# Kernel optimization log

Hardware: AMD Instinct MI355X
Metric: run time of the kernel (lower is better)

## Reference

```python
import jax, jax.numpy as jnp
import numpy as np

N_NODES = 100000
N_EDGES = 600000
F_IN = 128
HIDDEN = 128
Z_DIM = 64


def setup_inputs() -> dict:
    key = jax.random.key(0)
    ks = jax.random.split(key, 8)
    nodes = jax.random.normal(ks[0], (N_NODES, F_IN), dtype=jnp.float32)
    senders = jax.random.randint(ks[1], (N_EDGES,), 0, N_NODES, dtype=jnp.int32)
    receivers = jax.random.randint(ks[2], (N_EDGES,), 0, N_NODES, dtype=jnp.int32)
    s = lambda fan_in: 1.0 / np.sqrt(fan_in)
    W0 = jax.random.normal(ks[3], (F_IN, HIDDEN), dtype=jnp.float32) * s(F_IN)
    b0 = jnp.zeros((HIDDEN,), dtype=jnp.float32)
    W1 = jax.random.normal(ks[4], (HIDDEN, HIDDEN), dtype=jnp.float32) * s(HIDDEN)
    b1 = jnp.zeros((HIDDEN,), dtype=jnp.float32)
    Wmu = jax.random.normal(ks[5], (HIDDEN + F_IN, Z_DIM), dtype=jnp.float32) * s(HIDDEN + F_IN)
    bmu = jnp.zeros((Z_DIM,), dtype=jnp.float32)
    Wls = jax.random.normal(ks[6], (HIDDEN + F_IN, Z_DIM), dtype=jnp.float32) * s(HIDDEN + F_IN)
    bls = jnp.zeros((Z_DIM,), dtype=jnp.float32)
    return dict(nodes=nodes, senders=senders, receivers=receivers,
                W0=W0, b0=b0, W1=W1, b1=b1, Wmu=Wmu, bmu=bmu, Wls=Wls, bls=bls)


def _gc_layer(h, senders, receivers, W, b):
    """jraph.GraphConvolution with symmetric normalization, no self edges.
    update_node_fn = softmax(relu(Dense(h)))."""
    n = h.shape[0]
    h = jax.nn.softmax(jax.nn.relu(h @ W + b), axis=-1)  # [N, H]
    ones = jnp.ones_like(senders, dtype=h.dtype)
    sender_deg = jax.ops.segment_sum(ones, senders, num_segments=n)    # [N]
    receiver_deg = jax.ops.segment_sum(ones, receivers, num_segments=n)
    h = h * jax.lax.rsqrt(jnp.maximum(sender_deg, 1.0))[:, None]
    h = jax.ops.segment_sum(h[senders], receivers, num_segments=n)     # scatter-aggregate
    h = h * jax.lax.rsqrt(jnp.maximum(receiver_deg, 1.0))[:, None]
    return h


def reference(nodes, senders, receivers, W0, b0, W1, b1, Wmu, bmu, Wls, bls):
    h = _gc_layer(nodes, senders, receivers, W0, b0)
    h = _gc_layer(h, senders, receivers, W1, b1)
    h = jnp.concatenate([h, nodes], axis=-1)  # [N, HIDDEN + F_IN]
    mu = h @ Wmu + bmu
    logsig2 = h @ Wls + bls
    return (mu, logsig2)
```

## Files before the change

kernel.cpp:

```cpp
#include <hip/hip_runtime.h>

#define N_NODES 100000
#define N_EDGES 600000

#define NBUCK 391
#define BROWS 512
#define NCHUNK 128
#define V4_TOTAL (N_EDGES / 4)
#define V4_CHUNK ((V4_TOTAL + NCHUNK - 1) / NCHUNK)

typedef __attribute__((ext_vector_type(8))) short short8;
typedef __attribute__((ext_vector_type(4))) float f32x4;

__device__ inline unsigned short bf16r(float x) {
    unsigned u = __float_as_uint(x);
    return (unsigned short)((u + 0x7FFFu + ((u >> 16) & 1u)) >> 16);
}
__device__ inline unsigned bf16pack2(float x, float y) {
    unsigned ux = __float_as_uint(x), uy = __float_as_uint(y);
    ux = (ux + 0x7FFFu + ((ux >> 16) & 1u)) >> 16;
    uy = (uy + 0x7FFFu + ((uy >> 16) & 1u)) >> 16;
    return ux | (uy << 16);
}

__global__ void prep_weights(const float* __restrict__ W0, const float* __restrict__ W1,
                             const float* __restrict__ Wmu, const float* __restrict__ Wls,
                             unsigned short* __restrict__ w0t, unsigned short* __restrict__ w1t,
                             unsigned short* __restrict__ wht) {
    int i = blockIdx.x * 256 + threadIdx.x;
    if (i < 16384) {
        int nn = i >> 7, k = i & 127;
        w0t[i] = bf16r(W0[k * 128 + nn]);
    } else if (i < 32768) {
        int j = i - 16384;
        int nn = j >> 7, k = j & 127;
        w1t[j] = bf16r(W1[k * 128 + nn]);
    } else {
        int j = i - 32768;
        int nn = j >> 8, k = j & 255;
        float v = (nn < 64) ? Wmu[k * 64 + nn] : Wls[k * 64 + (nn - 64)];
        wht[j] = bf16r(v);
    }
}

__global__ __launch_bounds__(1024)
void bucket_hist(const int* __restrict__ receivers, const int* __restrict__ senders,
                 int* __restrict__ hR, int* __restrict__ hS) {
    __shared__ int cR[BROWS], cS[BROWS];
    const int t = threadIdx.x;
    if (t < BROWS) { cR[t] = 0; cS[t] = 0; }
    __syncthreads();
    const int v0 = blockIdx.x * V4_CHUNK;
    const int v1 = min(v0 + V4_CHUNK, V4_TOTAL);
    for (int i = v0 + t; i < v1; i += 1024) {
        const int4 r = ((const int4*)receivers)[i];
        const int4 s = ((const int4*)senders)[i];
        atomicAdd(&cR[r.x >> 8], 1); atomicAdd(&cR[r.y >> 8], 1);
        atomicAdd(&cR[r.z >> 8], 1); atomicAdd(&cR[r.w >> 8], 1);
        atomicAdd(&cS[s.x >> 8], 1); atomicAdd(&cS[s.y >> 8], 1);
        atomicAdd(&cS[s.z >> 8], 1); atomicAdd(&cS[s.w >> 8], 1);
    }
    __syncthreads();
    if (t < BROWS) {
        hR[blockIdx.x * BROWS + t] = cR[t];
        hS[blockIdx.x * BROWS + t] = cS[t];
    }
}

__global__ __launch_bounds__(512)
void bucket_scan(int* __restrict__ hR, int* __restrict__ hS,
                 int* __restrict__ baseR, int* __restrict__ baseS) {
    __shared__ int a[BROWS], b[BROWS], a2[BROWS], b2[BROWS];
    const int t = threadIdx.x;
    int totR = 0, totS = 0;
    for (int blk = 0; blk < NCHUNK; ++blk) {
        totR += hR[blk * BROWS + t];
        totS += hS[blk * BROWS + t];
    }
    a[t] = totR; a2[t] = totS;
    __syncthreads();
    int* pin = a; int* pout = b; int* qin = a2; int* qout = b2;
    for (int off = 1; off < BROWS; off <<= 1) {
        pout[t] = pin[t] + ((t >= off) ? pin[t - off] : 0);
        qout[t] = qin[t] + ((t >= off) ? qin[t - off] : 0);
        __syncthreads();
        int* tmp = pin; pin = pout; pout = tmp;
        tmp = qin; qin = qout; qout = tmp;
    }
    const int bR = pin[t] - totR;
    const int bS = qin[t] - totS;
    if (t <= NBUCK) { baseR[t] = (t == NBUCK) ? N_EDGES : bR; }
    if (t <= NBUCK) { baseS[t] = (t == NBUCK) ? N_EDGES : bS; }
    int curR = bR, curS = bS;
    for (int blk = 0; blk < NCHUNK; ++blk) {
        const int vR = hR[blk * BROWS + t]; hR[blk * BROWS + t] = curR; curR += vR;
        const int vS = hS[blk * BROWS + t]; hS[blk * BROWS + t] = curS; curS += vS;
    }
}

__global__ __launch_bounds__(1024)
void bucket_scatter(const int* __restrict__ receivers, const int* __restrict__ senders,
                    const int* __restrict__ hR, const int* __restrict__ hS,
                    uint2* __restrict__ pairs, int* __restrict__ sbuf) {
    __shared__ int cR[BROWS], cS[BROWS];
    const int t = threadIdx.x;
    if (t < BROWS) {
        cR[t] = hR[blockIdx.x * BROWS + t];
        cS[t] = hS[blockIdx.x * BROWS + t];
    }
    __syncthreads();
    const int v0 = blockIdx.x * V4_CHUNK;
    const int v1 = min(v0 + V4_CHUNK, V4_TOTAL);
    for (int i = v0 + t; i < v1; i += 1024) {
        const int4 r = ((const int4*)receivers)[i];
        const int4 s = ((const int4*)senders)[i];
        int p;
        p = atomicAdd(&cR[r.x >> 8], 1); pairs[p] = make_uint2((unsigned)r.x, (unsigned)s.x);
        p = atomicAdd(&cR[r.y >> 8], 1); pairs[p] = make_uint2((unsigned)r.y, (unsigned)s.y);
        p = atomicAdd(&cR[r.z >> 8], 1); pairs[p] = make_uint2((unsigned)r.z, (unsigned)s.z);
        p = atomicAdd(&cR[r.w >> 8], 1); pairs[p] = make_uint2((unsigned)r.w, (unsigned)s.w);
        p = atomicAdd(&cS[s.x >> 8], 1); sbuf[p] = s.x;
        p = atomicAdd(&cS[s.y >> 8], 1); sbuf[p] = s.y;
        p = atomicAdd(&cS[s.z >> 8], 1); sbuf[p] = s.z;
        p = atomicAdd(&cS[s.w >> 8], 1); sbuf[p] = s.w;
    }
}

__global__ __launch_bounds__(256)
void bucket_finalize(const uint2* __restrict__ pairs, const int* __restrict__ baseR,
                     int* __restrict__ offs, int* __restrict__ srt,
                     float* __restrict__ inv_r, int n) {
    __shared__ int cnt[256], cur[256];
    __shared__ int sa[256], sb[256];
    const int t = threadIdx.x;
    const int b = blockIdx.x;
    const int e0 = baseR[b], e1 = baseR[b + 1];
    cnt[t] = 0;
    __syncthreads();
    for (int i = e0 + t; i < e1; i += 256)
        atomicAdd(&cnt[pairs[i].x & 255u], 1);
    __syncthreads();
    const int v = cnt[t];
    sa[t] = v;
    __syncthreads();
    int* pin = sa; int* pout = sb;
    for (int off = 1; off < 256; off <<= 1) {
        pout[t] = pin[t] + ((t >= off) ? pin[t - off] : 0);
        __syncthreads();
        int* tmp = pin; pin = pout; pout = tmp;
    }
    cur[t] = pin[t] - v;
    const int node = (b << 8) + t;
    if (node < n) {
        offs[node] = e0 + pin[t] - v;
        inv_r[node] = rsqrtf(fmaxf((float)v, 1.0f));
    }
    if (b == 0 && t == 0) offs[n] = N_EDGES;
    __syncthreads();
    for (int i = e0 + t; i < e1; i += 256) {
        const uint2 pr = pairs[i];
        const int p = atomicAdd(&cur[pr.x & 255u], 1);
        srt[e0 + p] = (int)pr.y;
    }
}

__global__ __launch_bounds__(256)
void sender_count(const int* __restrict__ sbuf, const int* __restrict__ baseS,
                  float* __restrict__ inv_s, int n) {
    __shared__ int cnt[256];
    const int t = threadIdx.x;
    const int b = blockIdx.x;
    const int e0 = baseS[b], e1 = baseS[b + 1];
    cnt[t] = 0;
    __syncthreads();
    for (int i = e0 + t; i < e1; i += 256)
        atomicAdd(&cnt[sbuf[i] & 255], 1);
    __syncthreads();
    const int node = (b << 8) + t;
    if (node < n) inv_s[node] = rsqrtf(fmaxf((float)cnt[t], 1.0f));
}

__global__ __launch_bounds__(256)
void aggregate_kernel(const uint4* __restrict__ src, uint4* __restrict__ dst,
                      const int* __restrict__ offs, const int* __restrict__ srt,
                      const float* __restrict__ scale, int n) {
    const int lane = threadIdx.x & 63;
    const int wave = threadIdx.x >> 6;
    const int grp  = lane >> 4;
    const int l16  = lane & 15;
    const int wid  = blockIdx.x * 4 + wave;
    const int nwv  = gridDim.x * 4;
    const unsigned grpbase = lane & 48;

    for (int rb = wid * 4; rb < n; rb += nwv * 4) {
        const int r = rb + grp;
        const bool valid = (r < n);
        int beg = 0, deg = 0;
        if (valid) { beg = offs[r]; deg = offs[r + 1] - beg; }
        float ax[8];
        #pragma unroll
        for (int k = 0; k < 8; ++k) ax[k] = 0.0f;

        for (int j0 = 0; ; j0 += 16) {
            const int rem = deg - j0;
            int wm = rem;
            wm = max(wm, __shfl_xor(wm, 16));
            wm = max(wm, __shfl_xor(wm, 32));
            if (wm <= 0) break;
            const int idx = (j0 + l16 < deg) ? srt[beg + j0 + l16] : 0;
            const int jmax = (wm < 16) ? wm : 16;
            for (int j = 0; j < jmax; j += 8) {
                uint4 v[8];
                #pragma unroll
                for (int k = 0; k < 8; ++k) {
                    const int s = __shfl(idx, grpbase + j + k);
                    v[k] = make_uint4(0u, 0u, 0u, 0u);
                    if (j + k < rem) v[k] = src[(size_t)s * 16 + l16];
                }
                #pragma unroll
                for (int k = 0; k < 8; ++k) {
                    ax[0] += __uint_as_float(v[k].x << 16);
                    ax[1] += __uint_as_float(v[k].x & 0xFFFF0000u);
                    ax[2] += __uint_as_float(v[k].y << 16);
                    ax[3] += __uint_as_float(v[k].y & 0xFFFF0000u);
                    ax[4] += __uint_as_float(v[k].z << 16);
                    ax[5] += __uint_as_float(v[k].z & 0xFFFF0000u);
                    ax[6] += __uint_as_float(v[k].w << 16);
                    ax[7] += __uint_as_float(v[k].w & 0xFFFF0000u);
                }
            }
        }
        if (valid) {
            const float sc = scale[r];
            uint4 o;
            o.x = bf16pack2(ax[0] * sc, ax[1] * sc);
            o.y = bf16pack2(ax[2] * sc, ax[3] * sc);
            o.z = bf16pack2(ax[4] * sc, ax[5] * sc);
            o.w = bf16pack2(ax[6] * sc, ax[7] * sc);
            dst[(size_t)r * 16 + l16] = o;
        }
    }
}

template<bool IN_BF16>
__global__ __launch_bounds__(256)
void gc_mfma(const void* __restrict__ xv, const unsigned short* __restrict__ Wt,
             const float* __restrict__ bias, const float* __restrict__ inv_out,
             unsigned short* __restrict__ y, int nrows) {
    __shared__ unsigned short Xl[64 * 136];
    __shared__ float sred0[4][64];
    __shared__ float sred1[4][64];
    const int row0 = blockIdx.x * 64;
    if (IN_BF16) {
        const uint2* xs = (const uint2*)xv;
        for (int c = threadIdx.x; c < 64 * 32; c += 256) {
            int r = c >> 5, cu = c & 31;
            int grow = row0 + r;
            uint2 v = make_uint2(0u, 0u);
            if (grow < nrows) v = xs[(size_t)grow * 32 + cu];
            *((uint2*)&Xl[r * 136] + cu) = v;
        }
    } else {
        const float* x = (const float*)xv;
        for (int c = threadIdx.x; c < 64 * 32; c += 256) {
            int r = c >> 5, c4 = c & 31;
            int grow = row0 + r;
            float4 v = make_float4(0.f, 0.f, 0.f, 0.f);
            if (grow < nrows) v = *(const float4*)&x[(size_t)grow * 128 + c4 * 4];
            *(uint2*)&Xl[r * 136 + c4 * 4] = make_uint2(bf16pack2(v.x, v.y), bf16pack2(v.z, v.w));
        }
    }
    __syncthreads();

    const int lane = threadIdx.x & 63;
    const int w = threadIdx.x >> 6;
    const int q = lane >> 4;
    const int l16 = lane & 15;

    short8 bf[4][2];
    #pragma unroll
    for (int k0 = 0; k0 < 4; ++k0)
        #pragma unroll
        for (int nt = 0; nt < 2; ++nt) {
            int ncol = w * 32 + nt * 16 + l16;
            bf[k0][nt] = *(const short8*)&Wt[ncol * 128 + k0 * 32 + q * 8];
        }

    f32x4 acc[4][2] = {};
    #pragma unroll
    for (int k0 = 0; k0 < 4; ++k0) {
        #pragma unroll
        for (int m = 0; m < 4; ++m) {
            short8 a = *(const short8*)&Xl[(m * 16 + l16) * 136 + k0 * 32 + q * 8];
            acc[m][0] = __builtin_amdgcn_mfma_f32_16x16x32_bf16(a, bf[k0][0], acc[m][0], 0, 0, 0);
            acc[m][1] = __builtin_amdgcn_mfma_f32_16x16x32_bf16(a, bf[k0][1], acc[m][1], 0, 0, 0);
        }
    }

    const float bv0 = bias[w * 32 + l16];
    const float bv1 = bias[w * 32 + 16 + l16];
    float v[4][2][4];
    #pragma unroll
    for (int m = 0; m < 4; ++m)
        #pragma unroll
        for (int r = 0; r < 4; ++r) {
            v[m][0][r] = fmaxf(acc[m][0][r] + bv0, 0.0f);
            v[m][1][r] = fmaxf(acc[m][1][r] + bv1, 0.0f);
        }
    float t[4][4];
    #pragma unroll
    for (int m = 0; m < 4; ++m)
        #pragma unroll
        for (int r = 0; r < 4; ++r)
            t[m][r] = fmaxf(v[m][0][r], v[m][1][r]);
    #pragma unroll
    for (int off = 1; off < 16; off <<= 1)
        #pragma unroll
        for (int m = 0; m < 4; ++m)
            #pragma unroll
            for (int r = 0; r < 4; ++r)
                t[m][r] = fmaxf(t[m][r], __shfl_xor(t[m][r], off));
    if (l16 == 0) {
        #pragma unroll
        for (int m = 0; m < 4; ++m)
            #pragma unroll
            for (int r = 0; r < 4; ++r)
                sred0[w][m * 16 + q * 4 + r] = t[m][r];
    }
    __syncthreads();
    float M[4][4];
    #pragma unroll
    for (int m = 0; m < 4; ++m)
        #pragma unroll
        for (int r = 0; r < 4; ++r) {
            int row = m * 16 + q * 4 + r;
            M[m][r] = fmaxf(fmaxf(sred0[0][row], sred0[1][row]),
                            fmaxf(sred0[2][row], sred0[3][row]));
        }
    float s[4][4];
    #pragma unroll
    for (int m = 0; m < 4; ++m)
        #pragma unroll
        for (int r = 0; r < 4; ++r) {
            float e0 = __expf(v[m][0][r] - M[m][r]);
            float e1 = __expf(v[m][1][r] - M[m][r]);
            v[m][0][r] = e0; v[m][1][r] = e1;
            s[m][r] = e0 + e1;
        }
    #pragma unroll
    for (int off = 1; off < 16; off <<= 1)
        #pragma unroll
        for (int m = 0; m < 4; ++m)
            #pragma unroll
            for (int r = 0; r < 4; ++r)
                s[m][r] += __shfl_xor(s[m][r], off);
    if (l16 == 0) {
        #pragma unroll
        for (int m = 0; m < 4; ++m)
            #pragma unroll
            for (int r = 0; r < 4; ++r)
                sred1[w][m * 16 + q * 4 + r] = s[m][r];
    }
    __syncthreads();
    #pragma unroll
    for (int m = 0; m < 4; ++m)
        #pragma unroll
        for (int r = 0; r < 4; ++r) {
            int row = m * 16 + q * 4 + r;
            int grow = row0 + row;
            if (grow < nrows) {
                float S = sred1[0][row] + sred1[1][row] + sred1[2][row] + sred1[3][row];
                float sc = inv_out[grow] / S;
                unsigned short* yrow = &y[(size_t)grow * 128];
                yrow[w * 32 + l16]      = bf16r(v[m][0][r] * sc);
                yrow[w * 32 + 16 + l16] = bf16r(v[m][1][r] * sc);
            }
        }
}

__global__ __launch_bounds__(256)
void head_mfma(const unsigned short* __restrict__ h, const float* __restrict__ nodes,
               const unsigned short* __restrict__ Wt,
               const float* __restrict__ bmu, const float* __restrict__ bls,
               float* __restrict__ out, int nrows) {
    __shared__ unsigned short Xl[64 * 264];
    const int row0 = blockIdx.x * 64;
    {
        const uint2* hs = (const uint2*)h;
        for (int c = threadIdx.x; c < 64 * 32; c += 256) {
            int r = c >> 5, cu = c & 31;
            int grow = row0 + r;
            uint2 v = make_uint2(0u, 0u);
            if (grow < nrows) v = hs[(size_t)grow * 32 + cu];
            *((uint2*)&Xl[r * 264] + cu) = v;
        }
    }
    for (int c = threadIdx.x; c < 64 * 32; c += 256) {
        int r = c >> 5, c4 = c & 31;
        int grow = row0 + r;
        float4 v = make_float4(0.f, 0.f, 0.f, 0.f);
        if (grow < nrows) v = *(const float4*)&nodes[(size_t)grow * 128 + c4 * 4];
        *(uint2*)&Xl[r * 264 + 128 + c4 * 4] = make_uint2(bf16pack2(v.x, v.y), bf16pack2(v.z, v.w));
    }
    __syncthreads();

    const int lane = threadIdx.x & 63;
    const int w = threadIdx.x >> 6;
    const int q = lane >> 4;
    const int l16 = lane & 15;

    short8 bf[8][2];
    #pragma unroll
    for (int k0 = 0; k0 < 8; ++k0)
        #pragma unroll
        for (int nt = 0; nt < 2; ++nt) {
            int ncol = w * 32 + nt * 16 + l16;
            bf[k0][nt] = *(const short8*)&Wt[ncol * 256 + k0 * 32 + q * 8];
        }

    f32x4 acc[4][2] = {};
    #pragma unroll
    for (int k0 = 0; k0 < 8; ++k0) {
        #pragma unroll
        for (int m = 0; m < 4; ++m) {
            short8 a = *(const short8*)&Xl[(m * 16 + l16) * 264 + k0 * 32 + q * 8];
            acc[m][0] = __builtin_amdgcn_mfma_f32_16x16x32_bf16(a, bf[k0][0], acc[m][0], 0, 0, 0);
            acc[m][1] = __builtin_amdgcn_mfma_f32_16x16x32_bf16(a, bf[k0][1], acc[m][1], 0, 0, 0);
        }
    }

    const float* bb = (w < 2) ? bmu : bls;
    float* ob = (w < 2) ? out : out + (size_t)nrows * 64;
    const int c0 = (w & 1) * 32 + l16;
    const int c1 = c0 + 16;
    const float b0v = bb[c0], b1v = bb[c1];
    #pragma unroll
    for (int m = 0; m < 4; ++m)
        #pragma unroll
        for (int r = 0; r < 4; ++r) {
            int grow = row0 + m * 16 + q * 4 + r;
            if (grow < nrows) {
                ob[(size_t)grow * 64 + c0] = acc[m][0][r] + b0v;
                ob[(size_t)grow * 64 + c1] = acc[m][1][r] + b1v;
            }
        }
}

extern "C" void kernel_launch(void* const* d_in, const int* in_sizes, int n_in,
                              void* d_out, int out_size, void* d_ws, size_t ws_size,
                              hipStream_t stream) {
    const float* nodes     = (const float*)d_in[0];
    const int*   senders   = (const int*)d_in[1];
    const int*   receivers = (const int*)d_in[2];
    const float* W0  = (const float*)d_in[3];
    const float* b0  = (const float*)d_in[4];
    const float* W1  = (const float*)d_in[5];
    const float* b1  = (const float*)d_in[6];
    const float* Wmu = (const float*)d_in[7];
    const float* bmu = (const float*)d_in[8];
    const float* Wls = (const float*)d_in[9];
    const float* bls = (const float*)d_in[10];
    float* out = (float*)d_out;

    const int N = N_NODES;
    const int NT = (N + 63) / 64;

    float* inv_s = (float*)d_ws;
    float* inv_r = inv_s + N;
    unsigned short* buf0 = (unsigned short*)(inv_r + N);
    unsigned short* buf1 = buf0 + (size_t)N * 128;
    unsigned short* w0t  = buf1 + (size_t)N * 128;
    unsigned short* w1t  = w0t + 128 * 128;
    unsigned short* wht  = w1t + 128 * 128;

    int* offs = (int*)d_out;
    int* srt  = offs + (N + 1);

    uint2* pairs = (uint2*)buf0;
    int* sbuf  = (int*)(pairs + N_EDGES);
    int* hR    = sbuf + N_EDGES;
    int* hS    = hR + NCHUNK * BROWS;
    int* baseR = hS + NCHUNK * BROWS;
    int* baseS = baseR + 512;

    prep_weights<<<256, 256, 0, stream>>>(W0, W1, Wmu, Wls, w0t, w1t, wht);

    bucket_hist<<<NCHUNK, 1024, 0, stream>>>(receivers, senders, hR, hS);
    bucket_scan<<<1, 512, 0, stream>>>(hR, hS, baseR, baseS);
    bucket_scatter<<<NCHUNK, 1024, 0, stream>>>(receivers, senders, hR, hS, pairs, sbuf);
    bucket_finalize<<<NBUCK, 256, 0, stream>>>(pairs, baseR, offs, srt, inv_r, N);
    sender_count<<<NBUCK, 256, 0, stream>>>(sbuf, baseS, inv_s, N);

    gc_mfma<false><<<NT, 256, 0, stream>>>(nodes, w0t, b0, inv_s, buf0, N);
    aggregate_kernel<<<2048, 256, 0, stream>>>((const uint4*)buf0, (uint4*)buf1,
                                               offs, srt, inv_r, N);

    gc_mfma<true><<<NT, 256, 0, stream>>>(buf1, w1t, b1, inv_s, buf0, N);
    aggregate_kernel<<<2048, 256, 0, stream>>>((const uint4*)buf0, (uint4*)buf1,
                                               offs, srt, inv_r, N);

    head_mfma<<<NT, 256, 0, stream>>>(buf1, nodes, wht, bmu, bls, out, N);
}
```

Before: 305.2 us.

## Give each wave full rows in gc_mfma so softmax stays inside the wave

```diff
diff --git a/kernel.cpp b/kernel.cpp
--- a/kernel.cpp
+++ b/kernel.cpp
@@ -248,9 +248,12 @@
              const float* __restrict__ bias, const float* __restrict__ inv_out,
              unsigned short* __restrict__ y, int nrows) {
     __shared__ unsigned short Xl[64 * 136];
-    __shared__ float sred0[4][64];
-    __shared__ float sred1[4][64];
+    __shared__ float sinv[64];
     const int row0 = blockIdx.x * 64;
+    if (threadIdx.x < 64) {
+        int grow = row0 + threadIdx.x;
+        sinv[threadIdx.x] = (grow < nrows) ? inv_out[grow] : 1.0f;
+    }
     if (IN_BF16) {
         const uint2* xs = (const uint2*)xv;
         for (int c = threadIdx.x; c < 64 * 32; c += 256) {
@@ -277,105 +280,57 @@
     const int q = lane >> 4;
     const int l16 = lane & 15;
 
-    short8 bf[4][2];
+    short8 af[4];
     #pragma unroll
     for (int k0 = 0; k0 < 4; ++k0)
-        #pragma unroll
-        for (int nt = 0; nt < 2; ++nt) {
-            int ncol = w * 32 + nt * 16 + l16;
-            bf[k0][nt] = *(const short8*)&Wt[ncol * 128 + k0 * 32 + q * 8];
-        }
-
-    f32x4 acc[4][2] = {};
-    #pragma unroll
-    for (int k0 = 0; k0 < 4; ++k0) {
-        #pragma unroll
-        for (int m = 0; m < 4; ++m) {
-            short8 a = *(const short8*)&Xl[(m * 16 + l16) * 136 + k0 * 32 + q * 8];
-            acc[m][0] = __builtin_amdgcn_mfma_f32_16x16x32_bf16(a, bf[k0][0], acc[m][0], 0, 0, 0);
-            acc[m][1] = __builtin_amdgcn_mfma_f32_16x16x32_bf16(a, bf[k0][1], acc[m][1], 0, 0, 0);
-        }
-    }
-
-    const float bv0 = bias[w * 32 + l16];
-    const float bv1 = bias[w * 32 + 16 + l16];
-    float v[4][2][4];
-    #pragma unroll
-    for (int m = 0; m < 4; ++m)
+        af[k0] = *(const short8*)&Xl[(w * 16 + l16) * 136 + k0 * 32 + q * 8];
+
+    f32x4 acc[8] = {};
+    #pragma unroll
+    for (int nt = 0; nt < 8; ++nt) {
+        #pragma unroll
+        for (int k0 = 0; k0 < 4; ++k0) {
+            short8 b = *(const short8*)&Wt[(nt * 16 + l16) * 128 + k0 * 32 + q * 8];
+            acc[nt] = __builtin_amdgcn_mfma_f32_16x16x32_bf16(af[k0], b, acc[nt], 0, 0, 0);
+        }
+    }
+
+    float e[8][4];
+    float s[4] = {0.f, 0.f, 0.f, 0.f};
+    #pragma unroll
+    for (int nt = 0; nt < 8; ++nt) {
+        const float bv = bias[nt * 16 + l16];
         #pragma unroll
         for (int r = 0; r < 4; ++r) {
-            v[m][0][r] = fmaxf(acc[m][0][r] + bv0, 0.0f);
-            v[m][1][r] = fmaxf(acc[m][1][r] + bv1, 0.0f);
-        }
-    float t[4][4];
-    #pragma unroll
-    for (int m = 0; m < 4; ++m)
+            float ev = __expf(fmaxf(acc[nt][r] + bv, 0.0f));
+            e[nt][r] = ev;
+            s[r] += ev;
+        }
+    }
+    #pragma unroll
+    for (int off = 1; off < 16; off <<= 1)
         #pragma unroll
         for (int r = 0; r < 4; ++r)
-            t[m][r] = fmaxf(v[m][0][r], v[m][1][r]);
-    #pragma unroll
-    for (int off = 1; off < 16; off <<= 1)
-        #pragma unroll
-        for (int m = 0; m < 4; ++m)
-            #pragma unroll
-            for (int r = 0; r < 4; ++r)
-                t[m][r] = fmaxf(t[m][r], __shfl_xor(t[m][r], off));
-    if (l16 == 0) {
-        #pragma unroll
-        for (int m = 0; m < 4; ++m)
-            #pragma unroll
-            for (int r = 0; r < 4; ++r)
-                sred0[w][m * 16 + q * 4 + r] = t[m][r];
-    }
-    __syncthreads();
-    float M[4][4];
-    #pragma unroll
-    for (int m = 0; m < 4; ++m)
-        #pragma unroll
-        for (int r = 0; r < 4; ++r) {
-            int row = m * 16 + q * 4 + r;
-            M[m][r] = fmaxf(fmaxf(sred0[0][row], sred0[1][row]),
-                            fmaxf(sred0[2][row], sred0[3][row]));
-        }
-    float s[4][4];
-    #pragma unroll
-    for (int m = 0; m < 4; ++m)
-        #pragma unroll
-        for (int r = 0; r < 4; ++r) {
-            float e0 = __expf(v[m][0][r] - M[m][r]);
-            float e1 = __expf(v[m][1][r] - M[m][r]);
-            v[m][0][r] = e0; v[m][1][r] = e1;
-            s[m][r] = e0 + e1;
-        }
-    #pragma unroll
-    for (int off = 1; off < 16; off <<= 1)
-        #pragma unroll
-        for (int m = 0; m < 4; ++m)
-            #pragma unroll
-            for (int r = 0; r < 4; ++r)
-                s[m][r] += __shfl_xor(s[m][r], off);
-    if (l16 == 0) {
-        #pragma unroll
-        for (int m = 0; m < 4; ++m)
-            #pragma unroll
-            for (int r = 0; r < 4; ++r)
-                sred1[w][m * 16 + q * 4 + r] = s[m][r];
-    }
-    __syncthreads();
-    #pragma unroll
-    for (int m = 0; m < 4; ++m)
-        #pragma unroll
-        for (int r = 0; r < 4; ++r) {
-            int row = m * 16 + q * 4 + r;
-            int grow = row0 + row;
-            if (grow < nrows) {
-                float S = sred1[0][row] + sred1[1][row] + sred1[2][row] + sred1[3][row];
-                float sc = inv_out[grow] / S;
-                unsigned short* yrow = &y[(size_t)grow * 128];
-                yrow[w * 32 + l16]      = bf16r(v[m][0][r] * sc);
-                yrow[w * 32 + 16 + l16] = bf16r(v[m][1][r] * sc);
-            }
-        }
+            s[r] += __shfl_xor(s[r], off);
+
+    #pragma unroll
+    for (int r = 0; r < 4; ++r) {
+        const int rl = w * 16 + q * 4 + r;
+        const float sc = sinv[rl] / s[r];
+        #pragma unroll
+        for (int nt = 0; nt < 8; ++nt)
+            Xl[rl * 136 + nt * 16 + l16] = bf16r(e[nt][r] * sc);
+    }
+    __syncthreads();
+
+    for (int c = threadIdx.x; c < 64 * 16; c += 256) {
+        int r = c >> 4, cu = c & 15;
+        int grow = row0 + r;
+        if (grow < nrows) {
+            uint4 vv = *(const uint4*)&Xl[r * 136 + cu * 8];
+            *(uint4*)&y[(size_t)grow * 128 + cu * 8] = vv;
+        }
+    }
 }
 
 __global__ __launch_bounds__(256)
```

Result: slower. 311.7 us (+2.1%).
